# Performance work log

Measured on AMD Instinct MI355X. Metric: run time of the kernel, lower is better.

## Reference

```python
import jax, jax.numpy as jnp
import numpy as np

NUM_HEADS = 16
HEAD_DIM = 64
MODEL_DIM = NUM_HEADS * HEAD_DIM  # 1024
N_TOKENS = 121
BATCH = 1024
DISTURB_HEADS = np.array([0, 3], dtype=int)


def setup_inputs() -> dict:
    key = jax.random.key(0)
    ks = jax.random.split(key, 8)
    scale = 1.0 / np.sqrt(MODEL_DIM)
    return {
        "query": jax.random.normal(ks[0], (BATCH, MODEL_DIM), dtype=jnp.float32),
        "key": jax.random.normal(ks[1], (BATCH, N_TOKENS, MODEL_DIM), dtype=jnp.float32),
        "value": jax.random.normal(ks[2], (BATCH, N_TOKENS, MODEL_DIM), dtype=jnp.float32),
        "Wq": jax.random.normal(ks[3], (MODEL_DIM, MODEL_DIM), dtype=jnp.float32) * scale,
        "bq": jnp.zeros((MODEL_DIM,), dtype=jnp.float32),
        "Wk": jax.random.normal(ks[4], (MODEL_DIM, MODEL_DIM), dtype=jnp.float32) * scale,
        "bk": jnp.zeros((MODEL_DIM,), dtype=jnp.float32),
        "Wv": jax.random.normal(ks[5], (MODEL_DIM, MODEL_DIM), dtype=jnp.float32) * scale,
        "bv": jnp.zeros((MODEL_DIM,), dtype=jnp.float32),
    }


def reference(query, key, value, Wq, bq, Wk, bk, Wv, bv):
    B, N, _ = key.shape
    H, d = NUM_HEADS, HEAD_DIM
    # Linear projections (plain GEMMs)
    q_proj = query @ Wq + bq            # [B, H*d]
    k_proj = key @ Wk + bk              # [B, N, H*d]
    v_proj = value @ Wv + bv            # [B, N, H*d]

    q = q_proj.reshape(B, H, d)         # [B, H, d]
    k = k_proj.reshape(B, N, H, d)      # [B, N, H, d]
    v = v_proj.reshape(B, N, H, d)

    # single-query scores per head: [B, H, N]
    scores = jnp.einsum('bhd,bnhd->bhn', q, k)
    # head-wise disturb override: masked heads get all-ones scores
    mask = jnp.zeros((H,), dtype=bool).at[DISTURB_HEADS].set(True)[None, :, None]
    scores = jnp.where(mask, jnp.ones_like(scores), scores)
    # note: original scales by sqrt(d * H), not sqrt(d)
    scores = scores / jnp.sqrt(jnp.asarray(d * H, dtype=scores.dtype))
    weights = jax.nn.softmax(scores, axis=-1)   # [B, H, N]
    output = jnp.einsum('bhn,bnhd->bhd', weights, v).reshape(B, H * d)
    return (output, weights)
```

## Files before the change

### kernel.cpp

```cpp
#include <hip/hip_runtime.h>
#include <hip/hip_bf16.h>

#define NHEADS 16
#define HDIM   64
#define MDIM   1024
#define NTOK   121
#define NBATCH 1024

typedef __attribute__((ext_vector_type(4))) float f32x4;
typedef __attribute__((ext_vector_type(4))) short s16x4;
typedef __attribute__((ext_vector_type(8))) short s16x8;

#define WAIT_VM(n)  asm volatile("s_waitcnt vmcnt(" #n ")" ::: "memory")
#define WAIT_LGKM0() asm volatile("s_waitcnt lgkmcnt(0)" ::: "memory")

__device__ __forceinline__ short f2bf(float f) {
  __hip_bfloat16 h = __float2bfloat16(f);
  return __builtin_bit_cast(short, h);
}

#define GLDS(gptr, lptr)                                                        \
  __builtin_amdgcn_global_load_lds(                                             \
      (const __attribute__((address_space(1))) void*)(gptr),                    \
      (__attribute__((address_space(3))) void*)(lptr), 16, 0, 0)

__global__ __launch_bounds__(256) void kTransW(const float* __restrict__ Wq,
                                               const float* __restrict__ Wk,
                                               const float* __restrict__ Wv,
                                               short* __restrict__ Wt) {
  int bid = blockIdx.x;
  int m = bid >> 8, tile = bid & 255;
  int tr = tile >> 4, tc = tile & 15;
  const float* W = (m == 0) ? Wq : (m == 1) ? Wk : Wv;
  short* T = Wt + (size_t)m * (MDIM * MDIM);
  __shared__ float tl[64][68];
  int t = threadIdx.x;
  int c4 = t & 15, r0 = t >> 4;
#pragma unroll
  for (int i = 0; i < 4; ++i) {
    int kr = r0 + i * 16;
    f32x4 v = *(const f32x4*)(W + (size_t)(tr * 64 + kr) * MDIM + tc * 64 + c4 * 4);
    *(f32x4*)&tl[kr][c4 * 4] = v;
  }
  __syncthreads();
#pragma unroll
  for (int i = 0; i < 4; ++i) {
    int n = r0 + i * 16;
    s16x4 o;
    o.x = f2bf(tl[c4 * 4 + 0][n]);
    o.y = f2bf(tl[c4 * 4 + 1][n]);
    o.z = f2bf(tl[c4 * 4 + 2][n]);
    o.w = f2bf(tl[c4 * 4 + 3][n]);
    *(s16x4*)(T + (size_t)(tc * 64 + n) * MDIM + tr * 64 + c4 * 4) = o;
  }
}

__device__ __forceinline__ void gemm_core(const float* __restrict__ A, int mrows,
                                          const short* __restrict__ Wt, int c0,
                                          short* Alds, short* Bl0, short* Bl1,
                                          f32x4 acc[4][4], int t) {
  int wid = t >> 6, lane = t & 63;
  int wr = wid >> 1, wc = wid & 1;
  int li = lane & 15, lg = lane >> 4;
  int kq = t & 15, r0s = t >> 4;
#pragma unroll
  for (int fm = 0; fm < 4; ++fm)
#pragma unroll
    for (int fn = 0; fn < 4; ++fn) acc[fm][fn] = (f32x4)0.0f;

  int rhi[4];
#pragma unroll
  for (int i = 0; i < 4; ++i) {
    int row = r0s + 64 + (i << 4);
    rhi[i] = row < mrows ? row : mrows - 1;
  }
#pragma unroll
  for (int i = 0; i < 4; ++i) {
    int cl = wid * 32 + i * 8 + (lane >> 3);
    int jg = (lane & 7) ^ (cl & 7);
    GLDS(Wt + (size_t)(c0 + cl) * MDIM + jg * 8, Bl0 + (wid * 32 + i * 8) * 64);
  }
  f32x4 rLo[4];
#pragma unroll
  for (int i = 0; i < 4; ++i)
    rLo[i] = *(const f32x4*)(A + (size_t)(r0s + (i << 4)) * MDIM + kq * 4);

  for (int kt = 0; kt < 16; ++kt) {
    int k0 = kt * 64;
    short* Bcur = (kt & 1) ? Bl1 : Bl0;
    short* Bnxt = (kt & 1) ? Bl0 : Bl1;
    int kn = (kt < 15) ? k0 + 64 : 0;

    f32x4 rHi[4];
#pragma unroll
    for (int i = 0; i < 4; ++i)
      rHi[i] = *(const f32x4*)(A + (size_t)rhi[i] * MDIM + k0 + kq * 4);

    WAIT_VM(4);
    __builtin_amdgcn_s_barrier();
#pragma unroll
    for (int i = 0; i < 4; ++i) {
      int row = r0s + (i << 4);
      s16x4 b4;
      b4.x = f2bf(rLo[i].x); b4.y = f2bf(rLo[i].y);
      b4.z = f2bf(rLo[i].z); b4.w = f2bf(rLo[i].w);
      int byte = (row * 128 + kq * 8) ^ ((row & 7) << 4);
      *(s16x4*)((char*)Alds + byte) = b4;
    }
#pragma unroll
    for (int i = 0; i < 4; ++i) {
      int cl = wid * 32 + i * 8 + (lane >> 3);
      int jg = (lane & 7) ^ (cl & 7);
      GLDS(Wt + (size_t)(c0 + cl) * MDIM + kn + jg * 8, Bnxt + (wid * 32 + i * 8) * 64);
    }
    WAIT_VM(4);
#pragma unroll
    for (int i = 0; i < 4; ++i) {
      int row = r0s + 64 + (i << 4);
      s16x4 b4;
      b4.x = f2bf(rHi[i].x); b4.y = f2bf(rHi[i].y);
      b4.z = f2bf(rHi[i].z); b4.w = f2bf(rHi[i].w);
      int byte = (row * 128 + kq * 8) ^ ((row & 7) << 4);
      *(s16x4*)((char*)Alds + byte) = b4;
    }
#pragma unroll
    for (int i = 0; i < 4; ++i)
      rLo[i] = *(const f32x4*)(A + (size_t)(r0s + (i << 4)) * MDIM + kn + kq * 4);

    WAIT_LGKM0();
    __builtin_amdgcn_s_barrier();
#pragma unroll
    for (int ks = 0; ks < 2; ++ks) {
      s16x8 af[4];
      int kb = ks * 64 + lg * 16;
#pragma unroll
      for (int fm = 0; fm < 4; ++fm) {
        int row = wr * 64 + fm * 16 + li;
        int byte = (row * 128 + kb) ^ ((row & 7) << 4);
        af[fm] = *(s16x8*)((char*)Alds + byte);
      }
#pragma unroll
      for (int fn = 0; fn < 4; ++fn) {
        int col = wc * 64 + fn * 16 + li;
        int byte = (col * 128 + kb) ^ ((col & 7) << 4);
        s16x8 bfv = *(s16x8*)((char*)Bcur + byte);
#pragma unroll
        for (int fm = 0; fm < 4; ++fm)
          acc[fm][fn] = __builtin_amdgcn_mfma_f32_16x16x32_bf16(af[fm], bfv,
                                                                acc[fm][fn], 0, 0, 0);
      }
    }
  }
}

__global__ __launch_bounds__(256, 3) void kQProj(const float* __restrict__ query,
                                                 const short* __restrict__ WtQ,
                                                 const float* __restrict__ bq,
                                                 float* __restrict__ qp) {
  __shared__ alignas(16) short Alds[128 * 64];
  __shared__ alignas(16) short Bl0[128 * 64];
  __shared__ alignas(16) short Bl1[128 * 64];
  int bid = blockIdx.x;
  int rt = bid >> 3, ct = bid & 7;
  f32x4 acc[4][4];
  int t = threadIdx.x;
  gemm_core(query + (size_t)rt * 128 * MDIM, 128, WtQ, ct * 128, Alds, Bl0, Bl1, acc, t);
  int wid = t >> 6, lane = t & 63;
  int wr = wid >> 1, wc = wid & 1, li = lane & 15, lg = lane >> 4;
#pragma unroll
  for (int fn = 0; fn < 4; ++fn) {
    int col = ct * 128 + wc * 64 + fn * 16 + li;
    float bqv = bq[col];
#pragma unroll
    for (int fm = 0; fm < 4; ++fm)
#pragma unroll
      for (int rr = 0; rr < 4; ++rr) {
        int row = rt * 128 + wr * 64 + fm * 16 + lg * 4 + rr;
        qp[(size_t)row * MDIM + col] = acc[fm][fn][rr] + bqv;
      }
  }
}

__global__ __launch_bounds__(256, 3) void kG(const float* __restrict__ qp,
                                             const short* __restrict__ WtK,
                                             short* __restrict__ g) {
  __shared__ alignas(16) short Alds[128 * 64];
  __shared__ alignas(16) short Blds[128 * 64];
  int bid = blockIdx.x;
  int h = bid >> 6, bt = (bid >> 3) & 7, it = bid & 7;
  int t = threadIdx.x;
  int wid = t >> 6, lane = t & 63;
  int wr = wid >> 1, wc = wid & 1, li = lane & 15, lg = lane >> 4;
  int kq = t & 15, r0s = t >> 4;
#pragma unroll
  for (int i = 0; i < 8; ++i) {
    int r = r0s + 16 * i;
    f32x4 v = *(const f32x4*)(qp + (size_t)(bt * 128 + r) * MDIM + h * 64 + kq * 4);
    s16x4 b4;
    b4.x = f2bf(v.x); b4.y = f2bf(v.y); b4.z = f2bf(v.z); b4.w = f2bf(v.w);
    int byte = (r * 128 + kq * 8) ^ ((r & 7) << 4);
    *(s16x4*)((char*)Alds + byte) = b4;
  }
  {
    int jr = t >> 2, qc = t & 3;
#pragma unroll
    for (int q = 0; q < 4; ++q) {
      s16x8 v = *(const s16x8*)(WtK + (size_t)(h * 64 + jr) * MDIM + it * 128 +
                                qc * 32 + q * 8);
#pragma unroll
      for (int e = 0; e < 8; ++e) {
        int i = qc * 32 + q * 8 + e;
        int byte = (i * 128 + jr * 2) ^ ((i & 7) << 4);
        *(short*)((char*)Blds + byte) = v[e];
      }
    }
  }
  __syncthreads();
  f32x4 acc[4][4];
#pragma unroll
  for (int fm = 0; fm < 4; ++fm)
#pragma unroll
    for (int fn = 0; fn < 4; ++fn) acc[fm][fn] = (f32x4)0.0f;
#pragma unroll
  for (int ks = 0; ks < 2; ++ks) {
    int kb = ks * 64 + lg * 16;
    s16x8 af[4];
#pragma unroll
    for (int fm = 0; fm < 4; ++fm) {
      int row = wr * 64 + fm * 16 + li;
      int byte = (row * 128 + kb) ^ ((row & 7) << 4);
      af[fm] = *(s16x8*)((char*)Alds + byte);
    }
#pragma unroll
    for (int fn = 0; fn < 4; ++fn) {
      int col = wc * 64 + fn * 16 + li;
      int byte = (col * 128 + kb) ^ ((col & 7) << 4);
      s16x8 bfv = *(s16x8*)((char*)Blds + byte);
#pragma unroll
      for (int fm = 0; fm < 4; ++fm)
        acc[fm][fn] = __builtin_amdgcn_mfma_f32_16x16x32_bf16(af[fm], bfv,
                                                              acc[fm][fn], 0, 0, 0);
    }
  }
#pragma unroll
  for (int fm = 0; fm < 4; ++fm)
#pragma unroll
    for (int rr = 0; rr < 4; ++rr) {
      int b = bt * 128 + wr * 64 + fm * 16 + lg * 4 + rr;
      short* gp = g + ((size_t)b * 16 + h) * 1024 + it * 128;
#pragma unroll
      for (int fn = 0; fn < 4; ++fn)
        gp[wc * 64 + fn * 16 + li] = f2bf(acc[fm][fn][rr]);
    }
}

__global__ __launch_bounds__(512) void kW(const float* __restrict__ key,
                                          const short* __restrict__ g,
                                          float* __restrict__ weights) {
  __shared__ alignas(16) short Kl0[128 * 64];
  __shared__ alignas(16) short Kl1[128 * 64];
  __shared__ alignas(16) short Glds[16 * 1024];
  __shared__ float s_lds[16][132];
  int b = blockIdx.x;
  int t = threadIdx.x;
  int wid = t >> 6, lane = t & 63, li = lane & 15, lg = lane >> 4;
  int kq = t & 15, r0s = t >> 4;
  int rcl[4];
#pragma unroll
  for (int i = 0; i < 4; ++i) {
    int r = r0s + 32 * i;
    rcl[i] = r < NTOK ? r : NTOK - 1;
  }
  const float* A = key + (size_t)b * NTOK * MDIM;
  const short* gb = g + (size_t)b * 16384;
#pragma unroll
  for (int q = 0; q < 4; ++q) {
    int c = q * 512 + t;
    s16x8 v = *(const s16x8*)(gb + c * 8);
    int byte = ((c >> 7) * 2048 + (c & 127) * 16) ^ (((c >> 7) & 7) << 4);
    *(s16x8*)((char*)Glds + byte) = v;
  }
  f32x4 rA0[4], rA1[4];
#pragma unroll
  for (int i = 0; i < 4; ++i)
    rA0[i] = *(const f32x4*)(A + (size_t)rcl[i] * MDIM + kq * 4);
#pragma unroll
  for (int i = 0; i < 4; ++i)
    rA1[i] = *(const f32x4*)(A + (size_t)rcl[i] * MDIM + 64 + kq * 4);
  WAIT_LGKM0();
  __builtin_amdgcn_s_barrier();
  f32x4 acc = (f32x4)0.0f;

  for (int kt = 0; kt < 16; kt += 2) {
    WAIT_VM(4);
#pragma unroll
    for (int i = 0; i < 4; ++i) {
      int row = r0s + 32 * i;
      s16x4 b4;
      b4.x = f2bf(rA0[i].x); b4.y = f2bf(rA0[i].y);
      b4.z = f2bf(rA0[i].z); b4.w = f2bf(rA0[i].w);
      int byte = (row * 128 + kq * 8) ^ ((row & 7) << 4);
      *(s16x4*)((char*)Kl0 + byte) = b4;
    }
    {
      int kn = (kt + 2 < 16) ? (kt + 2) * 64 : 0;
#pragma unroll
      for (int i = 0; i < 4; ++i)
        rA0[i] = *(const f32x4*)(A + (size_t)rcl[i] * MDIM + kn + kq * 4);
    }
    WAIT_LGKM0();
    __builtin_amdgcn_s_barrier();
#pragma unroll
    for (int ks = 0; ks < 2; ++ks) {
      int kb = ks * 64 + lg * 16;
      int row = wid * 16 + li;
      s16x8 af = *(s16x8*)((char*)Kl0 + ((row * 128 + kb) ^ ((row & 7) << 4)));
      int kel = kt * 64 + ks * 32 + lg * 8;
      s16x8 bf = *(s16x8*)((char*)Glds + ((li * 2048 + kel * 2) ^ ((li & 7) << 4)));
      acc = __builtin_amdgcn_mfma_f32_16x16x32_bf16(af, bf, acc, 0, 0, 0);
    }
    WAIT_VM(4);
#pragma unroll
    for (int i = 0; i < 4; ++i) {
      int row = r0s + 32 * i;
      s16x4 b4;
      b4.x = f2bf(rA1[i].x); b4.y = f2bf(rA1[i].y);
      b4.z = f2bf(rA1[i].z); b4.w = f2bf(rA1[i].w);
      int byte = (row * 128 + kq * 8) ^ ((row & 7) << 4);
      *(s16x4*)((char*)Kl1 + byte) = b4;
    }
    {
      int kn = (kt + 3 < 16) ? (kt + 3) * 64 : 64;
#pragma unroll
      for (int i = 0; i < 4; ++i)
        rA1[i] = *(const f32x4*)(A + (size_t)rcl[i] * MDIM + kn + kq * 4);
    }
    WAIT_LGKM0();
    __builtin_amdgcn_s_barrier();
#pragma unroll
    for (int ks = 0; ks < 2; ++ks) {
      int kb = ks * 64 + lg * 16;
      int row = wid * 16 + li;
      s16x8 af = *(s16x8*)((char*)Kl1 + ((row * 128 + kb) ^ ((row & 7) << 4)));
      int kel = (kt + 1) * 64 + ks * 32 + lg * 8;
      s16x8 bf = *(s16x8*)((char*)Glds + ((li * 2048 + kel * 2) ^ ((li & 7) << 4)));
      acc = __builtin_amdgcn_mfma_f32_16x16x32_bf16(af, bf, acc, 0, 0, 0);
    }
  }
#pragma unroll
  for (int rr = 0; rr < 4; ++rr) s_lds[li][wid * 16 + lg * 4 + rr] = acc[rr];
  __syncthreads();
#pragma unroll
  for (int hh = 0; hh < 2; ++hh) {
    int h = wid * 2 + hh;
    int n0 = lane, n1 = lane + 64;
    bool v0 = (n0 < NTOK), v1 = (n1 < NTOK);
    float w0, w1;
    if (h == 0 || h == 3) {
      w0 = 1.f / NTOK; w1 = 1.f / NTOK;
    } else {
      const float kinv = 1.f / 32.f;
      float s0 = v0 ? s_lds[h][n0] * kinv : -1e30f;
      float s1 = v1 ? s_lds[h][n1] * kinv : -1e30f;
      float m = fmaxf(s0, s1);
#pragma unroll
      for (int msk = 1; msk < 64; msk <<= 1) m = fmaxf(m, __shfl_xor(m, msk));
      float e0 = v0 ? __expf(s0 - m) : 0.f;
      float e1 = v1 ? __expf(s1 - m) : 0.f;
      float s = e0 + e1;
#pragma unroll
      for (int msk = 1; msk < 64; msk <<= 1) s += __shfl_xor(s, msk);
      float inv = 1.f / s;
      w0 = e0 * inv; w1 = e1 * inv;
    }
    float* wp = weights + ((size_t)b * NHEADS + h) * NTOK;
    if (v0) wp[n0] = w0;
    if (v1) wp[n1] = w1;
  }
}

__global__ __launch_bounds__(512, 4) void kV(const float* __restrict__ value,
                                             const float* __restrict__ weights,
                                             short* __restrict__ vbar) {
  __shared__ float w_lds[16][128];
  int b = blockIdx.x;
  int t = threadIdx.x;
  int grp = t >> 7, ic = t & 127;
#pragma unroll
  for (int q = 0; q < 4; ++q) {
    int idx = q * 512 + t;
    int h = idx >> 7, n = idx & 127;
    w_lds[h][n] = (n < NTOK) ? weights[((size_t)b * NHEADS + h) * NTOK + n] : 0.f;
  }
  __syncthreads();
  const float* V = value + (size_t)b * NTOK * MDIM;
  f32x4 a0[4], a1[4];
#pragma unroll
  for (int hh = 0; hh < 4; ++hh) { a0[hh] = (f32x4)0.0f; a1[hh] = (f32x4)0.0f; }
#pragma unroll 4
  for (int n = 0; n < NTOK; ++n) {
    f32x4 v0 = *(const f32x4*)(V + (size_t)n * MDIM + ic * 8);
    f32x4 v1 = *(const f32x4*)(V + (size_t)n * MDIM + ic * 8 + 4);
#pragma unroll
    for (int hh = 0; hh < 4; ++hh) {
      float wn = w_lds[grp * 4 + hh][n];
      a0[hh] += wn * v0;
      a1[hh] += wn * v1;
    }
  }
#pragma unroll
  for (int hh = 0; hh < 4; ++hh) {
    s16x8 o;
    o[0] = f2bf(a0[hh].x); o[1] = f2bf(a0[hh].y);
    o[2] = f2bf(a0[hh].z); o[3] = f2bf(a0[hh].w);
    o[4] = f2bf(a1[hh].x); o[5] = f2bf(a1[hh].y);
    o[6] = f2bf(a1[hh].z); o[7] = f2bf(a1[hh].w);
    *(s16x8*)(vbar + ((size_t)b * 16 + grp * 4 + hh) * 1024 + ic * 8) = o;
  }
}

__global__ __launch_bounds__(256, 3) void kO(const short* __restrict__ vbar,
                                             const short* __restrict__ WtV,
                                             const float* __restrict__ bv,
                                             float* __restrict__ outp) {
  __shared__ alignas(16) short Alds[128 * 64];
  __shared__ alignas(16) short Blds[64 * 64];
  int bid = blockIdx.x;
  int bt = bid >> 4, h = bid & 15;
  int t = threadIdx.x;
  int wid = t >> 6, lane = t & 63;
  int wr = wid >> 1, wc = wid & 1, li = lane & 15, lg = lane >> 4;
  f32x4 acc[4][2];
#pragma unroll
  for (int fm = 0; fm < 4; ++fm)
#pragma unroll
    for (int fn = 0; fn < 2; ++fn) acc[fm][fn] = (f32x4)0.0f;

  for (int kt = 0; kt < 16; ++kt) {
    int k0 = kt * 64;
    __syncthreads();
#pragma unroll
    for (int i = 0; i < 4; ++i) {
      int lrow = wid * 32 + i * 8 + (lane >> 3);
      int jg = (lane & 7) ^ (lrow & 7);
      GLDS(vbar + ((size_t)(bt * 128 + lrow) * 16 + h) * 1024 + k0 + jg * 8,
           Alds + (wid * 32 + i * 8) * 64);
    }
#pragma unroll
    for (int j = 0; j < 2; ++j) {
      int cl = wid * 16 + j * 8 + (lane >> 3);
      int jg = (lane & 7) ^ (cl & 7);
      GLDS(WtV + (size_t)(h * 64 + cl) * MDIM + k0 + jg * 8,
           Blds + (wid * 16 + j * 8) * 64);
    }
    __syncthreads();
#pragma unroll
    for (int ks = 0; ks < 2; ++ks) {
      int kb = ks * 64 + lg * 16;
      s16x8 af[4];
#pragma unroll
      for (int fm = 0; fm < 4; ++fm) {
        int row = wr * 64 + fm * 16 + li;
        int byte = (row * 128 + kb) ^ ((row & 7) << 4);
        af[fm] = *(s16x8*)((char*)Alds + byte);
      }
#pragma unroll
      for (int fn = 0; fn < 2; ++fn) {
        int col = wc * 32 + fn * 16 + li;
        int byte = (col * 128 + kb) ^ ((col & 7) << 4);
        s16x8 bfv = *(s16x8*)((char*)Blds + byte);
#pragma unroll
        for (int fm = 0; fm < 4; ++fm)
          acc[fm][fn] = __builtin_amdgcn_mfma_f32_16x16x32_bf16(af[fm], bfv,
                                                                acc[fm][fn], 0, 0, 0);
      }
    }
  }
#pragma unroll
  for (int fn = 0; fn < 2; ++fn) {
    int cg = h * 64 + wc * 32 + fn * 16 + li;
    float bvv = bv[cg];
#pragma unroll
    for (int fm = 0; fm < 4; ++fm)
#pragma unroll
      for (int rr = 0; rr < 4; ++rr) {
        int row = bt * 128 + wr * 64 + fm * 16 + lg * 4 + rr;
        outp[(size_t)row * MDIM + cg] = acc[fm][fn][rr] + bvv;
      }
  }
}

extern "C" void kernel_launch(void* const* d_in, const int* in_sizes, int n_in,
                              void* d_out, int out_size, void* d_ws, size_t ws_size,
                              hipStream_t stream) {
  const float* query = (const float*)d_in[0];
  const float* key   = (const float*)d_in[1];
  const float* value = (const float*)d_in[2];
  const float* Wq    = (const float*)d_in[3];
  const float* bq    = (const float*)d_in[4];
  const float* Wk    = (const float*)d_in[5];
  const float* bk    = (const float*)d_in[6];
  const float* Wv    = (const float*)d_in[7];
  const float* bv    = (const float*)d_in[8];
  (void)bk;

  float* out     = (float*)d_out;
  float* weights = out + (size_t)NBATCH * MDIM;

  char* ws = (char*)d_ws;
  short* Wt   = (short*)ws;
  float* qp   = (float*)(ws + 6u  * 1024 * 1024);
  short* g    = (short*)(ws + 10u * 1024 * 1024);
  short* vbar = (short*)(ws + 48u * 1024 * 1024);

  kTransW<<<dim3(768),  dim3(256), 0, stream>>>(Wq, Wk, Wv, Wt);
  kQProj <<<dim3(64),   dim3(256), 0, stream>>>(query, Wt, bq, qp);
  kG     <<<dim3(1024), dim3(256), 0, stream>>>(qp, Wt + (size_t)MDIM * MDIM, g);
  kW     <<<dim3(1024), dim3(512), 0, stream>>>(key, g, weights);
  kV     <<<dim3(1024), dim3(512), 0, stream>>>(value, weights, vbar);
  kO     <<<dim3(128),  dim3(256), 0, stream>>>(vbar, Wt + 2 * (size_t)MDIM * MDIM,
                                                bv, out);
}
```

Baseline: 315.0 us.

## Stream G tiles into a small ring buffer in kW and batch V loads in kV

In kW, the full 32KB per-batch G tile in LDS is replaced by a 4-slot ring of 2KB chunks. Two waves fill the ring with global_load_lds, pipelined alongside the key prefetch, and the score buffer now reuses Kl0. The smaller LDS footprint is meant to let more blocks fit per CU (launch bounds raised to 6). In kV, the token loop loads 8 rows of V at once to increase memory-level parallelism, at the cost of more registers and more complex per-wave vmcnt bookkeeping.

Measured after the change: 342.9 us. 1.09x slower.

```diff
diff --git a/kernel.cpp b/kernel.cpp
--- a/kernel.cpp
+++ b/kernel.cpp
@@ -254,13 +254,12 @@
     }
 }
 
-__global__ __launch_bounds__(512) void kW(const float* __restrict__ key,
-                                          const short* __restrict__ g,
-                                          float* __restrict__ weights) {
+__global__ __launch_bounds__(512, 6) void kW(const float* __restrict__ key,
+                                             const short* __restrict__ g,
+                                             float* __restrict__ weights) {
   __shared__ alignas(16) short Kl0[128 * 64];
   __shared__ alignas(16) short Kl1[128 * 64];
-  __shared__ alignas(16) short Glds[16 * 1024];
-  __shared__ float s_lds[16][132];
+  __shared__ alignas(16) short Gl[4][1024];
   int b = blockIdx.x;
   int t = threadIdx.x;
   int wid = t >> 6, lane = t & 63, li = lane & 15, lg = lane >> 4;
@@ -273,26 +272,23 @@
   }
   const float* A = key + (size_t)b * NTOK * MDIM;
   const short* gb = g + (size_t)b * 16384;
-#pragma unroll
-  for (int q = 0; q < 4; ++q) {
-    int c = q * 512 + t;
-    s16x8 v = *(const s16x8*)(gb + c * 8);
-    int byte = ((c >> 7) * 2048 + (c & 127) * 16) ^ (((c >> 7) & 7) << 4);
-    *(s16x8*)((char*)Glds + byte) = v;
-  }
+  int gh = (wid & 1) * 8 + (lane >> 3);
+  int gc = (((lane & 7) ^ (gh & 7)) * 8);
+
   f32x4 rA0[4], rA1[4];
 #pragma unroll
   for (int i = 0; i < 4; ++i)
     rA0[i] = *(const f32x4*)(A + (size_t)rcl[i] * MDIM + kq * 4);
+  if (wid < 2) GLDS(gb + gh * 1024 + 0 + gc, &Gl[0][wid * 512]);
 #pragma unroll
   for (int i = 0; i < 4; ++i)
     rA1[i] = *(const f32x4*)(A + (size_t)rcl[i] * MDIM + 64 + kq * 4);
-  WAIT_LGKM0();
-  __builtin_amdgcn_s_barrier();
+  if (wid < 2) GLDS(gb + gh * 1024 + 64 + gc, &Gl[1][wid * 512]);
   f32x4 acc = (f32x4)0.0f;
 
+#pragma unroll
   for (int kt = 0; kt < 16; kt += 2) {
-    WAIT_VM(4);
+    if (wid < 2) { WAIT_VM(6); } else { WAIT_VM(4); }
 #pragma unroll
     for (int i = 0; i < 4; ++i) {
       int row = r0s + 32 * i;
@@ -307,6 +303,10 @@
 #pragma unroll
       for (int i = 0; i < 4; ++i)
         rA0[i] = *(const f32x4*)(A + (size_t)rcl[i] * MDIM + kn + kq * 4);
+      if (wid < 2) {
+        GLDS(gb + gh * 1024 + kn + gc, &Gl[(kt + 2) & 3][wid * 512]);
+        WAIT_VM(10);
+      }
     }
     WAIT_LGKM0();
     __builtin_amdgcn_s_barrier();
@@ -315,11 +315,11 @@
       int kb = ks * 64 + lg * 16;
       int row = wid * 16 + li;
       s16x8 af = *(s16x8*)((char*)Kl0 + ((row * 128 + kb) ^ ((row & 7) << 4)));
-      int kel = kt * 64 + ks * 32 + lg * 8;
-      s16x8 bf = *(s16x8*)((char*)Glds + ((li * 2048 + kel * 2) ^ ((li & 7) << 4)));
+      s16x8 bf = *(s16x8*)((char*)&Gl[kt & 3][0] +
+                           ((li * 128 + ks * 64 + lg * 16) ^ ((li & 7) << 4)));
       acc = __builtin_amdgcn_mfma_f32_16x16x32_bf16(af, bf, acc, 0, 0, 0);
     }
-    WAIT_VM(4);
+    if (wid < 2) { WAIT_VM(6); } else { WAIT_VM(4); }
 #pragma unroll
     for (int i = 0; i < 4; ++i) {
       int row = r0s + 32 * i;
@@ -330,10 +330,14 @@
       *(s16x4*)((char*)Kl1 + byte) = b4;
     }
     {
-      int kn = (kt + 3 < 16) ? (kt + 3) * 64 : 64;
+      int kn = (kt + 3 < 16) ? (kt + 3) * 64 : 0;
 #pragma unroll
       for (int i = 0; i < 4; ++i)
         rA1[i] = *(const f32x4*)(A + (size_t)rcl[i] * MDIM + kn + kq * 4);
+      if (wid < 2) {
+        GLDS(gb + gh * 1024 + kn + gc, &Gl[(kt + 3) & 3][wid * 512]);
+        WAIT_VM(10);
+      }
     }
     WAIT_LGKM0();
     __builtin_amdgcn_s_barrier();
@@ -342,11 +346,12 @@
       int kb = ks * 64 + lg * 16;
       int row = wid * 16 + li;
       s16x8 af = *(s16x8*)((char*)Kl1 + ((row * 128 + kb) ^ ((row & 7) << 4)));
-      int kel = (kt + 1) * 64 + ks * 32 + lg * 8;
-      s16x8 bf = *(s16x8*)((char*)Glds + ((li * 2048 + kel * 2) ^ ((li & 7) << 4)));
+      s16x8 bf = *(s16x8*)((char*)&Gl[(kt + 1) & 3][0] +
+                           ((li * 128 + ks * 64 + lg * 16) ^ ((li & 7) << 4)));
       acc = __builtin_amdgcn_mfma_f32_16x16x32_bf16(af, bf, acc, 0, 0, 0);
     }
   }
+  float (*s_lds)[132] = (float(*)[132])Kl0;
 #pragma unroll
   for (int rr = 0; rr < 4; ++rr) s_lds[li][wid * 16 + lg * 4 + rr] = acc[rr];
   __syncthreads();
@@ -397,13 +402,29 @@
   f32x4 a0[4], a1[4];
 #pragma unroll
   for (int hh = 0; hh < 4; ++hh) { a0[hh] = (f32x4)0.0f; a1[hh] = (f32x4)0.0f; }
-#pragma unroll 4
-  for (int n = 0; n < NTOK; ++n) {
-    f32x4 v0 = *(const f32x4*)(V + (size_t)n * MDIM + ic * 8);
-    f32x4 v1 = *(const f32x4*)(V + (size_t)n * MDIM + ic * 8 + 4);
+#pragma unroll 1
+  for (int n0 = 0; n0 < 120; n0 += 8) {
+    f32x4 v[16];
+#pragma unroll
+    for (int j = 0; j < 8; ++j) {
+      v[2 * j]     = *(const f32x4*)(V + (size_t)(n0 + j) * MDIM + ic * 8);
+      v[2 * j + 1] = *(const f32x4*)(V + (size_t)(n0 + j) * MDIM + ic * 8 + 4);
+    }
+#pragma unroll
+    for (int j = 0; j < 8; ++j)
+#pragma unroll
+      for (int hh = 0; hh < 4; ++hh) {
+        float wn = w_lds[grp * 4 + hh][n0 + j];
+        a0[hh] += wn * v[2 * j];
+        a1[hh] += wn * v[2 * j + 1];
+      }
+  }
+  {
+    f32x4 v0 = *(const f32x4*)(V + (size_t)120 * MDIM + ic * 8);
+    f32x4 v1 = *(const f32x4*)(V + (size_t)120 * MDIM + ic * 8 + 4);
 #pragma unroll
     for (int hh = 0; hh < 4; ++hh) {
-      float wn = w_lds[grp * 4 + hh][n];
+      float wn = w_lds[grp * 4 + hh][120];
       a0[hh] += wn * v0;
       a1[hh] += wn * v1;
     }
```
